# Performance work log

Measured on AMD Instinct MI355X. Metric: run time of the kernel, lower is better.

## Reference

```python
import jax, jax.numpy as jnp
import numpy as np

EPS = 1e-5
H = 8  # num_heads

def _bn(x, g, b):
    # training-mode BatchNorm over the LAST axis as channels; stats over all other axes
    axes = tuple(range(x.ndim - 1))
    mean = jnp.mean(x, axis=axes)
    var = jnp.var(x, axis=axes)  # biased, matches torch BN normalization
    return (x - mean) * jax.lax.rsqrt(var + EPS) * g + b


def setup_inputs() -> dict:
    key = jax.random.key(0)
    ks = jax.random.split(key, 16)
    m, S, C = 256, 128, 256
    s = 1.0 / np.sqrt(C)
    inp = {
        'x': jax.random.normal(ks[0], (m, S, C), jnp.float32),
        'g_n': jnp.ones((C,), jnp.float32), 'b_n': jnp.zeros((C,), jnp.float32),
        'Wq': jax.random.normal(ks[1], (C, C), jnp.float32) * s,
        'Wk': jax.random.normal(ks[2], (C, C), jnp.float32) * s,
        'Wv': jax.random.normal(ks[3], (C, C), jnp.float32) * s,
        'Wo': jax.random.normal(ks[4], (C, C), jnp.float32) * s,
        'bo': jnp.zeros((C,), jnp.float32),
        'g_pe': jnp.ones((S * S,), jnp.float32), 'b_pe': jnp.zeros((S * S,), jnp.float32),
        'g0': jnp.ones((C,), jnp.float32), 'b0': jnp.zeros((C,), jnp.float32),
        'W0': jax.random.normal(ks[5], (2 * C, C), jnp.float32) * s,
        'g1': jnp.ones((2 * C,), jnp.float32), 'b1': jnp.zeros((2 * C,), jnp.float32),
        'W1': jax.random.normal(ks[6], (C, 2 * C), jnp.float32) * (1.0 / np.sqrt(2 * C)),
    }
    return inp


def reference(x, g_n, b_n, Wq, Wk, Wv, Wo, bo, g_pe, b_pe, g0, b0, W0, g1, b1, W1):
    m, S, C = x.shape
    d = C // H
    # --- SelfAttention ---
    h = _bn(x, g_n, b_n)  # BN over channels C, stats over (batch, seq)
    q = (h @ Wq.T).reshape(m, S, H, d)
    k = (h @ Wk.T).reshape(m, S, H, d)
    v = (h @ Wv.T).reshape(m, S, H, d)
    energy = jnp.einsum('nqhc,nkhc->nhqk', q, k)  # [m,H,S,S]
    # BatchNorm1d over the flattened S*S 'channel' axis, stats over (batch, heads)
    e = energy.reshape(m, H, S * S)
    e = _bn(e, g_pe, b_pe)
    energy_post = e.reshape(m, H, S, S)
    attn = jax.nn.softmax(energy_post / jnp.sqrt(jnp.float32(C)), axis=-1)
    o = jnp.einsum('nhql,nlhc->nqhc', attn, v).reshape(m, S, C)
    x1 = o @ Wo.T + bo + x  # residual
    # --- FFN block ---
    out0 = _bn(x1, g0, b0)
    out1 = jax.nn.relu(out0)
    out2 = out1 @ W0.T            # [m,S,2C]
    out3 = _bn(out2, g1, b1)
    out4 = jax.nn.relu(out3)
    out5 = out4 @ W1.T            # [m,S,C]
    return x1 + out5  # dropout p=0.0 -> identity
```

## Files before the change

kernel.cpp:

```cpp
#include <hip/hip_runtime.h>
#include <hip/hip_bf16.h>

#define HH 8
#define SS 128
#define CC 256
#define DD 32
#define NTOK 32768
#define NHB 2048
#define BNEPS 1e-5f

using bf16 = __hip_bfloat16;
typedef float f32x4 __attribute__((ext_vector_type(4)));
typedef __bf16 bf16x8 __attribute__((ext_vector_type(8)));

__device__ __forceinline__ bf16x8 ld8(const bf16* p) {
    return *reinterpret_cast<const bf16x8*>(p);
}
__device__ __forceinline__ f32x4 ldf4(const float* p) {
    return *reinterpret_cast<const f32x4*>(p);
}
__device__ __forceinline__ void st8(bf16* p, bf16x8 v) {
    *reinterpret_cast<bf16x8*>(p) = v;
}
__device__ __forceinline__ bf16 bfc(__bf16 x) {
    union { __bf16 i; bf16 o; } u;
    u.i = x;
    return u.o;
}
__device__ __forceinline__ int swzg(int row, int g) {
    return ((g & 8) | ((g & 7) ^ (row & 7))) << 3;
}

typedef __attribute__((address_space(1))) const void g_void;
typedef __attribute__((address_space(3))) void l_void;
__device__ __forceinline__ void gload_lds16(const bf16* g, bf16* l) {
    __builtin_amdgcn_global_load_lds((g_void*)g, (l_void*)l, 16, 0, 0);
}

__global__ __launch_bounds__(256) void prep(const float* __restrict__ wq,
                                            const float* __restrict__ wk,
                                            const float* __restrict__ wv,
                                            const float* __restrict__ wo,
                                            const float* __restrict__ w0,
                                            const float* __restrict__ w1,
                                            bf16* __restrict__ out,
                                            const float* __restrict__ X,
                                            float* __restrict__ part) {
    int tid = threadIdx.x;
    if (blockIdx.x < 512) {
        int i = (blockIdx.x * 256 + tid) * 4;
        const float* src;
        int off;
        if (i < 65536) { src = wq; off = i; }
        else if (i < 131072) { src = wk; off = i - 65536; }
        else if (i < 196608) { src = wv; off = i - 131072; }
        else if (i < 262144) { src = wo; off = i - 196608; }
        else if (i < 393216) { src = w0; off = i - 262144; }
        else { src = w1; off = i - 393216; }
        f32x4 v = ldf4(src + off);
#pragma unroll
        for (int u = 0; u < 4; u++) out[i + u] = __float2bfloat16(v[u]);
        return;
    }
    int bx = blockIdx.x - 512;
    int cv = tid & 63, slot = tid >> 6;
    int c0 = cv * 4;
    size_t row0 = (size_t)bx * 256 + slot;
    float s[4], s2[4];
#pragma unroll
    for (int u = 0; u < 4; u++) { s[u] = 0.f; s2[u] = 0.f; }
    for (int i = 0; i < 64; i++) {
        size_t row = row0 + (size_t)i * 4;
        f32x4 v = ldf4(X + row * 256 + c0);
#pragma unroll
        for (int u = 0; u < 4; u++) {
            float f = v[u];
            s[u] += f; s2[u] += f * f;
        }
    }
    __shared__ float red[256][8];
#pragma unroll
    for (int u = 0; u < 4; u++) {
        red[tid][u] = s[u];
        red[tid][4 + u] = s2[u];
    }
    __syncthreads();
    if (tid < 64) {
#pragma unroll
        for (int sl = 1; sl < 4; sl++)
#pragma unroll
            for (int u = 0; u < 4; u++) {
                s[u] += red[tid + sl * 64][u];
                s2[u] += red[tid + sl * 64][4 + u];
            }
        float* dst = part + (size_t)bx * 512;
#pragma unroll
        for (int u = 0; u < 4; u++) {
            dst[c0 + u] = s[u];
            dst[256 + c0 + u] = s2[u];
        }
    }
}

template <int CH, int P, int ROWS>
__global__ __launch_bounds__(256) void statsA_wide(const bf16* __restrict__ X,
                                                   float* __restrict__ part) {
    constexpr int RB = ROWS / P;
    int c0 = (blockIdx.x * 256 + threadIdx.x) * 8;
    size_t row0 = (size_t)blockIdx.y * RB;
    float s[8], s2[8];
#pragma unroll
    for (int u = 0; u < 8; u++) { s[u] = 0.f; s2[u] = 0.f; }
    for (int i = 0; i < RB; i++) {
        bf16x8 v = ld8(X + (row0 + i) * CH + c0);
#pragma unroll
        for (int u = 0; u < 8; u++) {
            float f = (float)v[u];
            s[u] += f; s2[u] += f * f;
        }
    }
    float* dst = part + (size_t)blockIdx.y * (2 * CH);
#pragma unroll
    for (int u = 0; u < 8; u++) {
        dst[c0 + u] = s[u];
        dst[CH + c0 + u] = s2[u];
    }
}

__global__ __launch_bounds__(256) void statsB(const float* __restrict__ part, int P,
                                              int nch, float inv_n, float ps,
                                              const float* __restrict__ gamma,
                                              const float* __restrict__ beta,
                                              float* __restrict__ scale,
                                              float* __restrict__ bias) {
    int cl = threadIdx.x & 63, sl = threadIdx.x >> 6;
    int c = blockIdx.x * 64 + cl;
    float s = 0.f, s2 = 0.f;
    for (int p = sl; p < P; p += 4) {
        s += part[(size_t)p * 2 * nch + c];
        s2 += part[(size_t)p * 2 * nch + nch + c];
    }
    __shared__ float red[2][4][64];
    red[0][sl][cl] = s;
    red[1][sl][cl] = s2;
    __syncthreads();
    if (threadIdx.x < 64) {
        s = red[0][0][cl] + red[0][1][cl] + red[0][2][cl] + red[0][3][cl];
        s2 = red[1][0][cl] + red[1][1][cl] + red[1][2][cl] + red[1][3][cl];
        float mean = s * inv_n;
        float var = s2 * inv_n - mean * mean;
        float rstd = rsqrtf(var + BNEPS);
        float sc = gamma[c] * rstd;
        scale[c] = sc * ps;
        bias[c] = (beta[c] - mean * sc) * ps;
    }
}

template <int MODE, bool STATS, int ASRC>
__device__ __forceinline__ void gemm_core(
    const bf16* __restrict__ A, const float* __restrict__ Af,
    const bf16* __restrict__ B, int m0, int n0, int N, int K,
    const float* __restrict__ a_scale, const float* __restrict__ a_bias,
    const float* __restrict__ bias, const float* __restrict__ resf,
    bf16* __restrict__ outb, float* __restrict__ outf, float* __restrict__ spart,
    char* smem) {
    bf16* As = (bf16*)smem;
    bf16* Bs = As + 128 * 64;
    int tid = threadIdx.x;
    int lane = tid & 63, wave = tid >> 6;
    int quad = lane >> 4, l16 = lane & 15;
    int wm = (wave >> 1) * 64, wn = (wave & 1) * 64;
    int srow = lane >> 3;
    int scol = (lane & 7) * 8;
    int sgc = (((lane & 7) ^ srow) << 3);
    const bf16* Ab = (ASRC == 0) ? A + (size_t)m0 * K : A;
    const bf16* Bb = B + (size_t)n0 * K;
    f32x4 acc[4][4];
#pragma unroll
    for (int i = 0; i < 4; i++)
#pragma unroll
        for (int j = 0; j < 4; j++) acc[i][j] = f32x4{0.f, 0.f, 0.f, 0.f};

    for (int kt = 0; kt < K; kt += 64) {
        if (kt) __syncthreads();
#pragma unroll
        for (int i = 0; i < 4; i++) {
            int r = i * 32 + wave * 8;
            gload_lds16(Bb + (size_t)(r + srow) * K + kt + sgc, Bs + r * 64);
        }
        if (ASRC == 0) {
#pragma unroll
            for (int i = 0; i < 4; i++) {
                int r = i * 32 + wave * 8;
                gload_lds16(Ab + (size_t)(r + srow) * K + kt + sgc, As + r * 64);
            }
        } else {
            int c = kt + scol;
            f32x4 s0 = ldf4(a_scale + c), s1 = ldf4(a_scale + c + 4);
            f32x4 b0 = ldf4(a_bias + c), b1 = ldf4(a_bias + c + 4);
#pragma unroll
            for (int i = 0; i < 4; i++) {
                int r = i * 32 + wave * 8;
                size_t row = (size_t)(m0 + r + srow);
                bf16x8 av;
                if (ASRC == 3) {
                    bf16x8 xv = ld8(Ab + row * K + c);
#pragma unroll
                    for (int u = 0; u < 4; u++) {
                        float f = (float)xv[u] * s0[u] + b0[u];
                        f = fmaxf(f, 0.f);
                        av[u] = (__bf16)__float2bfloat16(f);
                    }
#pragma unroll
                    for (int u = 0; u < 4; u++) {
                        float f = (float)xv[u + 4] * s1[u] + b1[u];
                        f = fmaxf(f, 0.f);
                        av[u + 4] = (__bf16)__float2bfloat16(f);
                    }
                } else {
                    f32x4 x0 = ldf4(Af + row * K + c), x1v = ldf4(Af + row * K + c + 4);
#pragma unroll
                    for (int u = 0; u < 4; u++) {
                        float f = x0[u] * s0[u] + b0[u];
                        if (ASRC == 2) f = fmaxf(f, 0.f);
                        av[u] = (__bf16)__float2bfloat16(f);
                    }
#pragma unroll
                    for (int u = 0; u < 4; u++) {
                        float f = x1v[u] * s1[u] + b1[u];
                        if (ASRC == 2) f = fmaxf(f, 0.f);
                        av[u + 4] = (__bf16)__float2bfloat16(f);
                    }
                }
                st8(As + (r + srow) * 64 + sgc, av);
            }
        }
        __syncthreads();
#pragma unroll
        for (int ks = 0; ks < 2; ks++) {
#pragma unroll
            for (int uu = 0; uu < 1; uu++) {}
            bf16x8 af[4], bfr[4];
            int gq = ks * 4 + quad;
            int kb_ = ((gq ^ (l16 & 7)) << 3);
#pragma unroll
            for (int i = 0; i < 4; i++)
                af[i] = ld8(As + (wm + i * 16 + l16) * 64 + kb_);
#pragma unroll
            for (int j = 0; j < 4; j++)
                bfr[j] = ld8(Bs + (wn + j * 16 + l16) * 64 + kb_);
#pragma unroll
            for (int i = 0; i < 4; i++)
#pragma unroll
                for (int j = 0; j < 4; j++)
                    acc[i][j] = __builtin_amdgcn_mfma_f32_16x16x32_bf16(
                        af[i], bfr[j], acc[i][j], 0, 0, 0);
        }
    }
    __syncthreads();

    if (MODE == 0) {
        bf16(*Ct)[136] = (bf16(*)[136])smem;
#pragma unroll
        for (int i = 0; i < 4; i++)
#pragma unroll
            for (int j = 0; j < 4; j++)
#pragma unroll
                for (int r = 0; r < 4; r++)
                    Ct[wm + i * 16 + quad * 4 + r][wn + j * 16 + l16] =
                        __float2bfloat16(acc[i][j][r]);
        __syncthreads();
        float s[8], s2[8];
        if (STATS) {
#pragma unroll
            for (int u = 0; u < 8; u++) { s[u] = 0.f; s2[u] = 0.f; }
        }
#pragma unroll
        for (int it = 0; it < 8; it++) {
            int idx = it * 256 + tid;
            int row = idx >> 4, colv = idx & 15;
            bf16x8 c = ld8(&Ct[row][colv * 8]);
            st8(outb + (size_t)(m0 + row) * N + n0 + colv * 8, c);
            if (STATS) {
#pragma unroll
                for (int u = 0; u < 8; u++) {
                    float f = (float)c[u];
                    s[u] += f; s2[u] += f * f;
                }
            }
        }
        if (STATS) {
            __syncthreads();
            float* rf = (float*)smem;
            int g = tid & 15, k = tid >> 4;
#pragma unroll
            for (int u = 0; u < 8; u++) {
                rf[(g * 16 + k) * 16 + u] = s[u];
                rf[(g * 16 + k) * 16 + 8 + u] = s2[u];
            }
            __syncthreads();
            if (tid < 16) {
                float a[8], b[8];
#pragma unroll
                for (int u = 0; u < 8; u++) { a[u] = 0.f; b[u] = 0.f; }
                for (int k2 = 0; k2 < 16; k2++)
#pragma unroll
                    for (int u = 0; u < 8; u++) {
                        a[u] += rf[(tid * 16 + k2) * 16 + u];
                        b[u] += rf[(tid * 16 + k2) * 16 + 8 + u];
                    }
                float* dst = spart + (size_t)(m0 >> 7) * 2 * N + n0 + tid * 8;
#pragma unroll
                for (int u = 0; u < 8; u++) {
                    dst[u] = a[u];
                    dst[N + u] = b[u];
                }
            }
        }
    } else {
        float(*Cf)[132] = (float(*)[132])smem;
        float s[4], s2[4];
        if (STATS) {
#pragma unroll
            for (int u = 0; u < 4; u++) { s[u] = 0.f; s2[u] = 0.f; }
        }
#pragma unroll
        for (int h = 0; h < 2; h++) {
            if (h) __syncthreads();
            if ((wm >> 6) == h) {
#pragma unroll
                for (int i = 0; i < 4; i++)
#pragma unroll
                    for (int j = 0; j < 4; j++)
#pragma unroll
                        for (int r = 0; r < 4; r++)
                            Cf[i * 16 + quad * 4 + r][wn + j * 16 + l16] = acc[i][j][r];
            }
            __syncthreads();
#pragma unroll
            for (int it = 0; it < 8; it++) {
                int idx = it * 256 + tid;
                int row = idx >> 5, cv = (idx & 31) * 4;
                f32x4 v = ldf4(&Cf[row][cv]);
                int gc = n0 + cv;
                size_t gi = (size_t)(m0 + h * 64 + row) * N + gc;
                f32x4 rr = ldf4(resf + gi);
                if (MODE == 1) {
                    f32x4 bb = ldf4(bias + gc);
                    v = v + bb + rr;
                } else {
                    v = v + rr;
                }
                *reinterpret_cast<f32x4*>(outf + gi) = v;
                if (STATS) {
#pragma unroll
                    for (int u = 0; u < 4; u++) {
                        s[u] += v[u]; s2[u] += v[u] * v[u];
                    }
                }
            }
        }
        if (STATS) {
            __syncthreads();
            float* rf = (float*)smem;
            int g = tid & 31, k = tid >> 5;
#pragma unroll
            for (int u = 0; u < 4; u++) {
                rf[(g * 8 + k) * 8 + u] = s[u];
                rf[(g * 8 + k) * 8 + 4 + u] = s2[u];
            }
            __syncthreads();
            if (tid < 32) {
                float a[4], b[4];
#pragma unroll
                for (int u = 0; u < 4; u++) { a[u] = 0.f; b[u] = 0.f; }
                for (int k2 = 0; k2 < 8; k2++)
#pragma unroll
                    for (int u = 0; u < 4; u++) {
                        a[u] += rf[(tid * 8 + k2) * 8 + u];
                        b[u] += rf[(tid * 8 + k2) * 8 + 4 + u];
                    }
                float* dst = spart + (size_t)(m0 >> 7) * 2 * N + n0 + tid * 4;
#pragma unroll
                for (int u = 0; u < 4; u++) {
                    dst[u] = a[u];
                    dst[N + u] = b[u];
                }
            }
        }
    }
}

template <int MODE, bool STATS, int ASRC>
__global__ __launch_bounds__(256) void gemm128(
    const bf16* __restrict__ A, const float* __restrict__ Af,
    const bf16* __restrict__ B, int N, int K, const float* __restrict__ a_scale,
    const float* __restrict__ a_bias, const float* __restrict__ bias,
    const float* __restrict__ resf, bf16* __restrict__ outb,
    float* __restrict__ outf, float* __restrict__ spart) {
    __shared__ __align__(16) char smem[34816];
    gemm_core<MODE, STATS, ASRC>(A, Af, B, blockIdx.x * 128, blockIdx.y * 128, N, K,
                                 a_scale, a_bias, bias, resf, outb, outf, spart, smem);
}

__global__ __launch_bounds__(256) void gemm_qkv128(const float* __restrict__ x,
                                                   const bf16* __restrict__ W,
                                                   const float* __restrict__ a_scale,
                                                   const float* __restrict__ a_bias,
                                                   bf16* __restrict__ qkv) {
    __shared__ __align__(16) char smem[34816];
    int mat = blockIdx.y >> 1;
    int n0 = (blockIdx.y & 1) * 128;
    gemm_core<0, false, 1>(nullptr, x, W + mat * 65536, blockIdx.x * 128, n0, CC, CC,
                           a_scale, a_bias, nullptr, nullptr,
                           qkv + (size_t)mat * 8388608, nullptr, nullptr, smem);
}

__global__ __launch_bounds__(256) void gemm_energy(const bf16* __restrict__ q,
                                                   const bf16* __restrict__ k,
                                                   bf16* __restrict__ E) {
    int nh = blockIdx.x;
    int nb = nh >> 3, hh = nh & 7;
    int tid = threadIdx.x;
    int lane = tid & 63, wave = tid >> 6;
    int quad = lane >> 4, l16 = lane & 15;
    int wm = (wave >> 1) * 64, wn = (wave & 1) * 64;
    size_t tb = (size_t)nb * SS;
    int cb = hh * DD + quad * 8;
    f32x4 zero = {0.f, 0.f, 0.f, 0.f};
    f32x4 acc[4][4];
#pragma unroll
    for (int i = 0; i < 4; i++)
#pragma unroll
        for (int j = 0; j < 4; j++) acc[i][j] = zero;
    bf16x8 af[4], bfg[4];
#pragma unroll
    for (int i = 0; i < 4; i++)
        af[i] = ld8(q + (tb + wm + i * 16 + l16) * CC + cb);
#pragma unroll
    for (int j = 0; j < 4; j++)
        bfg[j] = ld8(k + (tb + wn + j * 16 + l16) * CC + cb);
#pragma unroll
    for (int i = 0; i < 4; i++)
#pragma unroll
        for (int j = 0; j < 4; j++)
            acc[i][j] = __builtin_amdgcn_mfma_f32_16x16x32_bf16(af[i], bfg[j], acc[i][j], 0, 0, 0);
    __shared__ bf16 Et[128][136];
#pragma unroll
    for (int i = 0; i < 4; i++)
#pragma unroll
        for (int j = 0; j < 4; j++)
#pragma unroll
            for (int r = 0; r < 4; r++)
                Et[wm + i * 16 + quad * 4 + r][wn + j * 16 + l16] =
                    __float2bfloat16(acc[i][j][r]);
    __syncthreads();
    bf16* Eb = E + (size_t)nh * SS * SS;
#pragma unroll
    for (int it = 0; it < 8; it++) {
        int idx = it * 256 + tid;
        int row = idx >> 4, colv = idx & 15;
        st8(Eb + (size_t)row * SS + colv * 8, ld8(&Et[row][colv * 8]));
    }
}

__global__ __launch_bounds__(256, 4) void att_kernel(
    const bf16* __restrict__ E, const bf16* __restrict__ v,
    const float* __restrict__ pe_scale, const float* __restrict__ pe_bias,
    bf16* __restrict__ o) {
    __shared__ bf16 P[SS * 128];
    __shared__ bf16 Vt[DD * 128];
    int nh = blockIdx.x;
    int nb = nh >> 3, hh = nh & 7;
    const bf16* Eb = E + (size_t)nh * SS * SS;
    int tid = threadIdx.x;
    int wave = tid >> 6, lane = tid & 63;
    {
        int s = tid >> 1, d0 = (tid & 1) * 16;
        const bf16* vp = v + (size_t)(nb * SS + s) * CC + hh * DD + d0;
        bf16x8 v0 = ld8(vp), v1 = ld8(vp + 8);
        int g = s >> 3, sub = s & 7;
#pragma unroll
        for (int u = 0; u < 8; u++) {
            int da = d0 + u, db = d0 + 8 + u;
            Vt[da * 128 + swzg(da, g) + sub] = bfc(v0[u]);
            Vt[db * 128 + swzg(db, g) + sub] = bfc(v1[u]);
        }
    }
    int rs = lane >> 4, cg = lane & 15;
#pragma unroll
    for (int p = 0; p < 8; p++) {
        int r = wave * 32 + p * 4 + rs;
        int e8 = r * 128 + cg * 8;
        bf16x8 ev = ld8(Eb + e8);
        f32x4 s0 = ldf4(pe_scale + e8), s1 = ldf4(pe_scale + e8 + 4);
        f32x4 b0 = ldf4(pe_bias + e8), b1 = ldf4(pe_bias + e8 + 4);
        float l[8];
#pragma unroll
        for (int u = 0; u < 4; u++) l[u] = (float)ev[u] * s0[u] + b0[u];
#pragma unroll
        for (int u = 0; u < 4; u++) l[u + 4] = (float)ev[u + 4] * s1[u] + b1[u];
        float mx = fmaxf(fmaxf(fmaxf(l[0], l[1]), fmaxf(l[2], l[3])),
                         fmaxf(fmaxf(l[4], l[5]), fmaxf(l[6], l[7])));
#pragma unroll
        for (int off = 8; off; off >>= 1) mx = fmaxf(mx, __shfl_xor(mx, off, 16));
        float e[8], sm = 0.f;
#pragma unroll
        for (int u = 0; u < 8; u++) { e[u] = __expf(l[u] - mx); sm += e[u]; }
#pragma unroll
        for (int off = 8; off; off >>= 1) sm += __shfl_xor(sm, off, 16);
        float inv = 1.0f / sm;
        bf16x8 pv;
#pragma unroll
        for (int u = 0; u < 8; u++) pv[u] = (__bf16)__float2bfloat16(e[u] * inv);
        st8(&P[r * 128 + swzg(r, cg)], pv);
    }
    __syncthreads();
    int quad = lane >> 4, l16 = lane & 15;
    f32x4 acc[2][2];
#pragma unroll
    for (int i = 0; i < 2; i++)
#pragma unroll
        for (int j = 0; j < 2; j++) acc[i][j] = f32x4{0.f, 0.f, 0.f, 0.f};
#pragma unroll
    for (int kk = 0; kk < SS; kk += 32) {
        int g = (kk >> 3) + quad;
        int r0 = wave * 32 + l16, r1 = r0 + 16;
        bf16x8 a0 = ld8(&P[r0 * 128 + swzg(r0, g)]);
        bf16x8 a1 = ld8(&P[r1 * 128 + swzg(r1, g)]);
        bf16x8 b0 = ld8(&Vt[l16 * 128 + swzg(l16, g)]);
        bf16x8 b1 = ld8(&Vt[(l16 + 16) * 128 + swzg(l16 + 16, g)]);
        acc[0][0] = __builtin_amdgcn_mfma_f32_16x16x32_bf16(a0, b0, acc[0][0], 0, 0, 0);
        acc[0][1] = __builtin_amdgcn_mfma_f32_16x16x32_bf16(a0, b1, acc[0][1], 0, 0, 0);
        acc[1][0] = __builtin_amdgcn_mfma_f32_16x16x32_bf16(a1, b0, acc[1][0], 0, 0, 0);
        acc[1][1] = __builtin_amdgcn_mfma_f32_16x16x32_bf16(a1, b1, acc[1][1], 0, 0, 0);
    }
    __syncthreads();
    bf16* Ob = P;
#pragma unroll
    for (int i = 0; i < 2; i++)
#pragma unroll
        for (int j = 0; j < 2; j++)
#pragma unroll
            for (int r = 0; r < 4; r++) {
                int row = wave * 32 + i * 16 + quad * 4 + r;
                int col = j * 16 + l16;
                Ob[row * 40 + col] = __float2bfloat16(acc[i][j][r]);
            }
    __syncthreads();
#pragma unroll
    for (int it = 0; it < 2; it++) {
        int idx = it * 256 + tid;
        int row = idx >> 2, colv = idx & 3;
        st8(o + (size_t)(nb * SS + row) * CC + hh * DD + colv * 8,
            ld8(&Ob[row * 40 + colv * 8]));
    }
}

#define WB_OFF 0u
#define O_OFF 1048576u
#define Q_OFF 17825792u
#define K_OFF 34603008u
#define VT_OFF 51380224u
#define E_OFF 68157440u
#define X1_OFF 17825792u
#define OUT2_OFF 68157440u

extern "C" void kernel_launch(void* const* d_in, const int* in_sizes, int n_in,
                              void* d_out, int out_size, void* d_ws, size_t ws_size,
                              hipStream_t stream) {
    const float* x = (const float*)d_in[0];
    const float* g_n = (const float*)d_in[1];
    const float* b_n = (const float*)d_in[2];
    const float* Wq = (const float*)d_in[3];
    const float* Wk = (const float*)d_in[4];
    const float* Wv = (const float*)d_in[5];
    const float* Wo = (const float*)d_in[6];
    const float* bo = (const float*)d_in[7];
    const float* g_pe = (const float*)d_in[8];
    const float* b_pe = (const float*)d_in[9];
    const float* g0 = (const float*)d_in[10];
    const float* b0 = (const float*)d_in[11];
    const float* W0 = (const float*)d_in[12];
    const float* g1 = (const float*)d_in[13];
    const float* b1 = (const float*)d_in[14];
    const float* W1 = (const float*)d_in[15];

    char* ws = (char*)d_ws;
    bf16* WB = (bf16*)(ws + WB_OFF);
    bf16* WOB = WB + 196608;
    bf16* W0B = WB + 262144;
    bf16* W1B = WB + 393216;
    bf16* qb = (bf16*)(ws + Q_OFF);
    bf16* kb = (bf16*)(ws + K_OFF);
    bf16* vb = (bf16*)(ws + VT_OFF);
    bf16* Ebuf = (bf16*)(ws + E_OFF);
    bf16* obuf = (bf16*)(ws + O_OFF);
    float* x1 = (float*)(ws + X1_OFF);
    bf16* out2 = (bf16*)(ws + OUT2_OFF);
    float* bn1_scale = (float*)(ws + E_OFF);
    float* bn1_bias = bn1_scale + 256;
    float* xpart = (float*)(ws + E_OFF + 65536);
    float* pe_scale = (float*)(ws + Q_OFF);
    float* pe_bias = pe_scale + 16384;
    float* pepart = (float*)(ws + Q_OFF + 131072);
    float* bn0_scale = (float*)(ws + O_OFF);
    float* bn0_bias = bn0_scale + 256;
    float* f1_scale = (float*)(ws + O_OFF + 4096);
    float* f1_bias = f1_scale + 512;
    float* x1part = (float*)(ws + VT_OFF);
    float* f1part = (float*)(ws + O_OFF + 16384);
    float* outp = (float*)d_out;

    prep<<<640, 256, 0, stream>>>(Wq, Wk, Wv, Wo, W0, W1, WB, x, xpart);
    statsB<<<4, 256, 0, stream>>>(xpart, 128, 256, 1.0f / 32768.0f, 1.0f, g_n, b_n,
                                  bn1_scale, bn1_bias);
    gemm_qkv128<<<dim3(256, 6), 256, 0, stream>>>(x, WB, bn1_scale, bn1_bias, qb);
    gemm_energy<<<NHB, 256, 0, stream>>>(qb, kb, Ebuf);
    statsA_wide<16384, 32, 2048><<<dim3(8, 32), 256, 0, stream>>>(Ebuf, pepart);
    statsB<<<256, 256, 0, stream>>>(pepart, 32, 16384, 1.0f / 2048.0f, 0.0625f, g_pe,
                                    b_pe, pe_scale, pe_bias);
    att_kernel<<<NHB, 256, 0, stream>>>(Ebuf, vb, pe_scale, pe_bias, obuf);
    gemm128<1, true, 0><<<dim3(256, 2), 256, 0, stream>>>(
        obuf, nullptr, WOB, CC, CC, nullptr, nullptr, bo, x, nullptr, x1, x1part);
    statsB<<<4, 256, 0, stream>>>(x1part, 256, 256, 1.0f / 32768.0f, 1.0f, g0, b0,
                                  bn0_scale, bn0_bias);
    gemm128<0, true, 2><<<dim3(256, 4), 256, 0, stream>>>(
        nullptr, x1, W0B, 2 * CC, CC, bn0_scale, bn0_bias, nullptr, nullptr, out2,
        nullptr, f1part);
    statsB<<<8, 256, 0, stream>>>(f1part, 256, 512, 1.0f / 32768.0f, 1.0f, g1, b1,
                                  f1_scale, f1_bias);
    gemm128<2, false, 3><<<dim3(256, 2), 256, 0, stream>>>(
        out2, nullptr, W1B, CC, 2 * CC, f1_scale, f1_bias, nullptr, x1, nullptr, outp,
        nullptr);
    (void)in_sizes; (void)n_in; (void)out_size; (void)ws_size;
    (void)kb; (void)vb;
}
```

Baseline: 320.1 us.

## Prefetch next A tile into registers during MFMA compute in GEMM K-loop

Restructures the GEMM K-loop into a two-step unrolled loop. The global loads of the next A tile (the fp32 or bf16 activations that are normalized in registers) are issued before the current tile's MFMA compute, using ping-pong register buffers. This hides global load latency behind the matrix math. The cost is extra register pressure from the double-buffered A fragments, which may lower occupancy, and the loop assumes K is a multiple of 128.

```diff
diff --git a/kernel.cpp b/kernel.cpp
--- a/kernel.cpp
+++ b/kernel.cpp
@@ -181,81 +181,114 @@
 #pragma unroll
         for (int j = 0; j < 4; j++) acc[i][j] = f32x4{0.f, 0.f, 0.f, 0.f};
 
-    for (int kt = 0; kt < K; kt += 64) {
-        if (kt) __syncthreads();
+    f32x4 ax0_a[4], ax1_a[4], ax0_b[4], ax1_b[4];
+    bf16x8 ab_a[4], ab_b[4];
+
+    auto pfetchA = [&](int kt, f32x4 (&ax0)[4], f32x4 (&ax1)[4], bf16x8 (&ab)[4]) {
+        int c = kt + scol;
+#pragma unroll
+        for (int i = 0; i < 4; i++) {
+            size_t row = (size_t)(m0 + i * 32 + wave * 8 + srow);
+            if (ASRC == 3) {
+                ab[i] = ld8(Ab + row * K + c);
+            } else {
+                ax0[i] = ldf4(Af + row * K + c);
+                ax1[i] = ldf4(Af + row * K + c + 4);
+            }
+        }
+    };
+    auto stageA = [&](int kt, f32x4 (&ax0)[4], f32x4 (&ax1)[4], bf16x8 (&ab)[4]) {
+        int c = kt + scol;
+        f32x4 s0 = ldf4(a_scale + c), s1 = ldf4(a_scale + c + 4);
+        f32x4 b0 = ldf4(a_bias + c), b1 = ldf4(a_bias + c + 4);
+#pragma unroll
+        for (int i = 0; i < 4; i++) {
+            int r = i * 32 + wave * 8;
+            bf16x8 av;
+            if (ASRC == 3) {
+#pragma unroll
+                for (int u = 0; u < 4; u++) {
+                    float f = (float)ab[i][u] * s0[u] + b0[u];
+                    f = fmaxf(f, 0.f);
+                    av[u] = (__bf16)__float2bfloat16(f);
+                }
+#pragma unroll
+                for (int u = 0; u < 4; u++) {
+                    float f = (float)ab[i][u + 4] * s1[u] + b1[u];
+                    f = fmaxf(f, 0.f);
+                    av[u + 4] = (__bf16)__float2bfloat16(f);
+                }
+            } else {
+#pragma unroll
+                for (int u = 0; u < 4; u++) {
+                    float f = ax0[i][u] * s0[u] + b0[u];
+                    if (ASRC == 2) f = fmaxf(f, 0.f);
+                    av[u] = (__bf16)__float2bfloat16(f);
+                }
+#pragma unroll
+                for (int u = 0; u < 4; u++) {
+                    float f = ax1[i][u] * s1[u] + b1[u];
+                    if (ASRC == 2) f = fmaxf(f, 0.f);
+                    av[u + 4] = (__bf16)__float2bfloat16(f);
+                }
+            }
+            st8(As + (r + srow) * 64 + sgc, av);
+        }
+    };
+    auto computeK = [&]() {
+#pragma unroll
+        for (int ks = 0; ks < 2; ks++) {
+            bf16x8 af[4], bfr[4];
+            int gq = ks * 4 + quad;
+            int kb_ = ((gq ^ (l16 & 7)) << 3);
+#pragma unroll
+            for (int i = 0; i < 4; i++)
+                af[i] = ld8(As + (wm + i * 16 + l16) * 64 + kb_);
+#pragma unroll
+            for (int j = 0; j < 4; j++)
+                bfr[j] = ld8(Bs + (wn + j * 16 + l16) * 64 + kb_);
+#pragma unroll
+            for (int i = 0; i < 4; i++)
+#pragma unroll
+                for (int j = 0; j < 4; j++)
+                    acc[i][j] = __builtin_amdgcn_mfma_f32_16x16x32_bf16(
+                        af[i], bfr[j], acc[i][j], 0, 0, 0);
+        }
+    };
+    auto stageB = [&](int kt) {
 #pragma unroll
         for (int i = 0; i < 4; i++) {
             int r = i * 32 + wave * 8;
             gload_lds16(Bb + (size_t)(r + srow) * K + kt + sgc, Bs + r * 64);
         }
-        if (ASRC == 0) {
-#pragma unroll
-            for (int i = 0; i < 4; i++) {
-                int r = i * 32 + wave * 8;
-                gload_lds16(Ab + (size_t)(r + srow) * K + kt + sgc, As + r * 64);
-            }
-        } else {
-            int c = kt + scol;
-            f32x4 s0 = ldf4(a_scale + c), s1 = ldf4(a_scale + c + 4);
-            f32x4 b0 = ldf4(a_bias + c), b1 = ldf4(a_bias + c + 4);
-#pragma unroll
-            for (int i = 0; i < 4; i++) {
-                int r = i * 32 + wave * 8;
-                size_t row = (size_t)(m0 + r + srow);
-                bf16x8 av;
-                if (ASRC == 3) {
-                    bf16x8 xv = ld8(Ab + row * K + c);
-#pragma unroll
-                    for (int u = 0; u < 4; u++) {
-                        float f = (float)xv[u] * s0[u] + b0[u];
-                        f = fmaxf(f, 0.f);
-                        av[u] = (__bf16)__float2bfloat16(f);
-                    }
-#pragma unroll
-                    for (int u = 0; u < 4; u++) {
-                        float f = (float)xv[u + 4] * s1[u] + b1[u];
-                        f = fmaxf(f, 0.f);
-                        av[u + 4] = (__bf16)__float2bfloat16(f);
-                    }
-                } else {
-                    f32x4 x0 = ldf4(Af + row * K + c), x1v = ldf4(Af + row * K + c + 4);
-#pragma unroll
-                    for (int u = 0; u < 4; u++) {
-                        float f = x0[u] * s0[u] + b0[u];
-                        if (ASRC == 2) f = fmaxf(f, 0.f);
-                        av[u] = (__bf16)__float2bfloat16(f);
-                    }
-#pragma unroll
-                    for (int u = 0; u < 4; u++) {
-                        float f = x1v[u] * s1[u] + b1[u];
-                        if (ASRC == 2) f = fmaxf(f, 0.f);
-                        av[u + 4] = (__bf16)__float2bfloat16(f);
-                    }
-                }
-                st8(As + (r + srow) * 64 + sgc, av);
-            }
-        }
+    };
+    auto stageAdirect = [&](int kt) {
+#pragma unroll
+        for (int i = 0; i < 4; i++) {
+            int r = i * 32 + wave * 8;
+            gload_lds16(Ab + (size_t)(r + srow) * K + kt + sgc, As + r * 64);
+        }
+    };
+
+    if (ASRC != 0) pfetchA(0, ax0_a, ax1_a, ab_a);
+    int nsteps = K >> 6;
+    for (int t = 0; t < nsteps; t += 2) {
+        int kt0 = t << 6, kt1 = kt0 + 64;
+        if (kt0) __syncthreads();
+        stageB(kt0);
+        if (ASRC == 0) stageAdirect(kt0);
+        else stageA(kt0, ax0_a, ax1_a, ab_a);
         __syncthreads();
-#pragma unroll
-        for (int ks = 0; ks < 2; ks++) {
-#pragma unroll
-            for (int uu = 0; uu < 1; uu++) {}
-            bf16x8 af[4], bfr[4];
-            int gq = ks * 4 + quad;
-            int kb_ = ((gq ^ (l16 & 7)) << 3);
-#pragma unroll
-            for (int i = 0; i < 4; i++)
-                af[i] = ld8(As + (wm + i * 16 + l16) * 64 + kb_);
-#pragma unroll
-            for (int j = 0; j < 4; j++)
-                bfr[j] = ld8(Bs + (wn + j * 16 + l16) * 64 + kb_);
-#pragma unroll
-            for (int i = 0; i < 4; i++)
-#pragma unroll
-                for (int j = 0; j < 4; j++)
-                    acc[i][j] = __builtin_amdgcn_mfma_f32_16x16x32_bf16(
-                        af[i], bfr[j], acc[i][j], 0, 0, 0);
-        }
+        if (ASRC != 0) pfetchA(kt1, ax0_b, ax1_b, ab_b);
+        computeK();
+        __syncthreads();
+        stageB(kt1);
+        if (ASRC == 0) stageAdirect(kt1);
+        else stageA(kt1, ax0_b, ax1_b, ab_b);
+        __syncthreads();
+        if (ASRC != 0 && t + 2 < nsteps)
+            pfetchA(kt1 + 64, ax0_a, ax1_a, ab_a);
+        computeK();
     }
     __syncthreads();
 
```

Result: slower. 326.8 us (+2.1%).

## Widen projection GEMM tiles to full 256-column N so each block covers all outputs

Applied to the files above, without the earlier changes.

Replaces the 128x128 GEMM core with a full-width variant where each block computes all 256 output columns. QKV and W0 use 128x256 tiles with 512 threads, and Wo and W1 use 64x256 tiles with 256 threads. The aim is to read and BN-transform each A row only once instead of once per N tile, cutting redundant A loads and normalization work. The residual epilogue now writes straight from registers rather than staging through LDS, which gives less coalesced stores. The larger tiles and thread counts may also lower occupancy.

```diff
diff --git a/kernel.cpp b/kernel.cpp
--- a/kernel.cpp
+++ b/kernel.cpp
@@ -156,25 +156,26 @@
     }
 }
 
-template <int MODE, bool STATS, int ASRC>
-__device__ __forceinline__ void gemm_core(
+template <int WM, int MODE, int ASRC, bool STATS>
+__device__ __forceinline__ void gemm256_core(
     const bf16* __restrict__ A, const float* __restrict__ Af,
     const bf16* __restrict__ B, int m0, int n0, int N, int K,
     const float* __restrict__ a_scale, const float* __restrict__ a_bias,
     const float* __restrict__ bias, const float* __restrict__ resf,
     bf16* __restrict__ outb, float* __restrict__ outf, float* __restrict__ spart,
     char* smem) {
+    constexpr int BM = WM * 64;
+    constexpr int NT = WM * 256;
+    constexpr int NB = 8 / WM;
     bf16* As = (bf16*)smem;
-    bf16* Bs = As + 128 * 64;
+    bf16* Bs = As + BM * 64;
     int tid = threadIdx.x;
     int lane = tid & 63, wave = tid >> 6;
     int quad = lane >> 4, l16 = lane & 15;
-    int wm = (wave >> 1) * 64, wn = (wave & 1) * 64;
+    int wm = (wave >> 2) * 64, wn = (wave & 3) * 64;
     int srow = lane >> 3;
-    int scol = (lane & 7) * 8;
     int sgc = (((lane & 7) ^ srow) << 3);
-    const bf16* Ab = (ASRC == 0) ? A + (size_t)m0 * K : A;
-    const bf16* Bb = B + (size_t)n0 * K;
+    const bf16* Ab = A + (size_t)m0 * K;
     f32x4 acc[4][4];
 #pragma unroll
     for (int i = 0; i < 4; i++)
@@ -184,27 +185,28 @@
     for (int kt = 0; kt < K; kt += 64) {
         if (kt) __syncthreads();
 #pragma unroll
-        for (int i = 0; i < 4; i++) {
-            int r = i * 32 + wave * 8;
-            gload_lds16(Bb + (size_t)(r + srow) * K + kt + sgc, Bs + r * 64);
+        for (int i = 0; i < NB; i++) {
+            int r = i * (NT / 8) + wave * 8;
+            gload_lds16(B + (size_t)(r + srow) * K + kt + sgc, Bs + r * 64);
         }
         if (ASRC == 0) {
 #pragma unroll
-            for (int i = 0; i < 4; i++) {
-                int r = i * 32 + wave * 8;
+            for (int i = 0; i < 2; i++) {
+                int r = i * (BM / 2) + wave * 8;
                 gload_lds16(Ab + (size_t)(r + srow) * K + kt + sgc, As + r * 64);
             }
         } else {
-            int c = kt + scol;
-            f32x4 s0 = ldf4(a_scale + c), s1 = ldf4(a_scale + c + 4);
-            f32x4 b0 = ldf4(a_bias + c), b1 = ldf4(a_bias + c + 4);
-#pragma unroll
-            for (int i = 0; i < 4; i++) {
-                int r = i * 32 + wave * 8;
-                size_t row = (size_t)(m0 + r + srow);
+#pragma unroll
+            for (int c = 0; c < 2; c++) {
+                int flat = c * NT + tid;
+                int row = flat >> 3, sl = flat & 7;
+                int col = kt + sl * 8;
+                f32x4 s0 = ldf4(a_scale + col), s1 = ldf4(a_scale + col + 4);
+                f32x4 b0 = ldf4(a_bias + col), b1 = ldf4(a_bias + col + 4);
+                size_t grow = (size_t)(m0 + row);
                 bf16x8 av;
                 if (ASRC == 3) {
-                    bf16x8 xv = ld8(Ab + row * K + c);
+                    bf16x8 xv = ld8(A + grow * K + col);
 #pragma unroll
                     for (int u = 0; u < 4; u++) {
                         float f = (float)xv[u] * s0[u] + b0[u];
@@ -218,7 +220,8 @@
                         av[u + 4] = (__bf16)__float2bfloat16(f);
                     }
                 } else {
-                    f32x4 x0 = ldf4(Af + row * K + c), x1v = ldf4(Af + row * K + c + 4);
+                    f32x4 x0 = ldf4(Af + grow * K + col);
+                    f32x4 x1v = ldf4(Af + grow * K + col + 4);
 #pragma unroll
                     for (int u = 0; u < 4; u++) {
                         float f = x0[u] * s0[u] + b0[u];
@@ -232,14 +235,12 @@
                         av[u + 4] = (__bf16)__float2bfloat16(f);
                     }
                 }
-                st8(As + (r + srow) * 64 + sgc, av);
+                st8(As + row * 64 + ((sl ^ (row & 7)) << 3), av);
             }
         }
         __syncthreads();
 #pragma unroll
         for (int ks = 0; ks < 2; ks++) {
-#pragma unroll
-            for (int uu = 0; uu < 1; uu++) {}
             bf16x8 af[4], bfr[4];
             int gq = ks * 4 + quad;
             int kb_ = ((gq ^ (l16 & 7)) << 3);
@@ -261,159 +262,163 @@
 
     if (MODE == 0) {
         bf16(*Ct)[136] = (bf16(*)[136])smem;
+        float s[2][8], s2[2][8];
+        if (STATS) {
+#pragma unroll
+            for (int h = 0; h < 2; h++)
+#pragma unroll
+                for (int u = 0; u < 8; u++) { s[h][u] = 0.f; s2[h][u] = 0.f; }
+        }
+#pragma unroll
+        for (int h = 0; h < 2; h++) {
+            if (h) __syncthreads();
+            if ((wn >> 7) == h) {
+#pragma unroll
+                for (int i = 0; i < 4; i++)
+#pragma unroll
+                    for (int j = 0; j < 4; j++)
+#pragma unroll
+                        for (int r = 0; r < 4; r++)
+                            Ct[wm + i * 16 + quad * 4 + r]
+                              [(wn & 127) + j * 16 + l16] =
+                                __float2bfloat16(acc[i][j][r]);
+            }
+            __syncthreads();
+#pragma unroll
+            for (int it = 0; it < 4; it++) {
+                int idx = it * NT + tid;
+                int row = idx >> 4, colv = tid & 15;
+                bf16x8 c = ld8(&Ct[row][colv * 8]);
+                st8(outb + (size_t)(m0 + row) * N + n0 + h * 128 + colv * 8, c);
+                if (STATS) {
+#pragma unroll
+                    for (int u = 0; u < 8; u++) {
+                        float f = (float)c[u];
+                        s[h][u] += f; s2[h][u] += f * f;
+                    }
+                }
+            }
+        }
+        if (STATS) {
+            float* sc = (float*)smem;
+#pragma unroll
+            for (int h = 0; h < 2; h++) {
+                __syncthreads();
+#pragma unroll
+                for (int u = 0; u < 8; u++) {
+                    sc[tid * 16 + u] = s[h][u];
+                    sc[tid * 16 + 8 + u] = s2[h][u];
+                }
+                __syncthreads();
+                if (tid < 128) {
+                    int cv = tid >> 3, u = tid & 7;
+                    float a = 0.f, b = 0.f;
+                    for (int k = 0; k < NT / 16; k++) {
+                        a += sc[(k * 16 + cv) * 16 + u];
+                        b += sc[(k * 16 + cv) * 16 + 8 + u];
+                    }
+                    int ch = n0 + h * 128 + cv * 8 + u;
+                    spart[(size_t)blockIdx.x * 2 * N + ch] = a;
+                    spart[(size_t)blockIdx.x * 2 * N + N + ch] = b;
+                }
+            }
+        }
+    } else {
+        float bo4[4];
+        if (MODE == 1) {
+#pragma unroll
+            for (int j = 0; j < 4; j++) bo4[j] = bias[wn + j * 16 + l16];
+        }
+        float s[4], s2[4];
+        if (STATS) {
+#pragma unroll
+            for (int j = 0; j < 4; j++) { s[j] = 0.f; s2[j] = 0.f; }
+        }
 #pragma unroll
         for (int i = 0; i < 4; i++)
 #pragma unroll
             for (int j = 0; j < 4; j++)
 #pragma unroll
-                for (int r = 0; r < 4; r++)
-                    Ct[wm + i * 16 + quad * 4 + r][wn + j * 16 + l16] =
-                        __float2bfloat16(acc[i][j][r]);
-        __syncthreads();
-        float s[8], s2[8];
-        if (STATS) {
-#pragma unroll
-            for (int u = 0; u < 8; u++) { s[u] = 0.f; s2[u] = 0.f; }
-        }
-#pragma unroll
-        for (int it = 0; it < 8; it++) {
-            int idx = it * 256 + tid;
-            int row = idx >> 4, colv = idx & 15;
-            bf16x8 c = ld8(&Ct[row][colv * 8]);
-            st8(outb + (size_t)(m0 + row) * N + n0 + colv * 8, c);
-            if (STATS) {
-#pragma unroll
-                for (int u = 0; u < 8; u++) {
-                    float f = (float)c[u];
-                    s[u] += f; s2[u] += f * f;
+                for (int r = 0; r < 4; r++) {
+                    int rg = m0 + i * 16 + quad * 4 + r;
+                    int col = wn + j * 16 + l16;
+                    size_t gi = (size_t)rg * 256 + col;
+                    float v = acc[i][j][r] + resf[gi];
+                    if (MODE == 1) v += bo4[j];
+                    outf[gi] = v;
+                    if (STATS) { s[j] += v; s2[j] += v * v; }
                 }
-            }
-        }
         if (STATS) {
             __syncthreads();
-            float* rf = (float*)smem;
-            int g = tid & 15, k = tid >> 4;
-#pragma unroll
-            for (int u = 0; u < 8; u++) {
-                rf[(g * 16 + k) * 16 + u] = s[u];
-                rf[(g * 16 + k) * 16 + 8 + u] = s2[u];
+            float* sc = (float*)smem;
+#pragma unroll
+            for (int j = 0; j < 4; j++) {
+                sc[tid * 8 + j] = s[j];
+                sc[tid * 8 + 4 + j] = s2[j];
             }
             __syncthreads();
-            if (tid < 16) {
-                float a[8], b[8];
-#pragma unroll
-                for (int u = 0; u < 8; u++) { a[u] = 0.f; b[u] = 0.f; }
-                for (int k2 = 0; k2 < 16; k2++)
-#pragma unroll
-                    for (int u = 0; u < 8; u++) {
-                        a[u] += rf[(tid * 16 + k2) * 16 + u];
-                        b[u] += rf[(tid * 16 + k2) * 16 + 8 + u];
-                    }
-                float* dst = spart + (size_t)(m0 >> 7) * 2 * N + n0 + tid * 8;
-#pragma unroll
-                for (int u = 0; u < 8; u++) {
-                    dst[u] = a[u];
-                    dst[N + u] = b[u];
+            {
+                int w = tid >> 6, j = (tid >> 4) & 3, l = tid & 15;
+                float a = 0.f, b = 0.f;
+#pragma unroll
+                for (int q = 0; q < 4; q++) {
+                    a += sc[(w * 64 + q * 16 + l) * 8 + j];
+                    b += sc[(w * 64 + q * 16 + l) * 8 + 4 + j];
                 }
-            }
-        }
-    } else {
-        float(*Cf)[132] = (float(*)[132])smem;
-        float s[4], s2[4];
-        if (STATS) {
-#pragma unroll
-            for (int u = 0; u < 4; u++) { s[u] = 0.f; s2[u] = 0.f; }
-        }
-#pragma unroll
-        for (int h = 0; h < 2; h++) {
-            if (h) __syncthreads();
-            if ((wm >> 6) == h) {
-#pragma unroll
-                for (int i = 0; i < 4; i++)
-#pragma unroll
-                    for (int j = 0; j < 4; j++)
-#pragma unroll
-                        for (int r = 0; r < 4; r++)
-                            Cf[i * 16 + quad * 4 + r][wn + j * 16 + l16] = acc[i][j][r];
-            }
-            __syncthreads();
-#pragma unroll
-            for (int it = 0; it < 8; it++) {
-                int idx = it * 256 + tid;
-                int row = idx >> 5, cv = (idx & 31) * 4;
-                f32x4 v = ldf4(&Cf[row][cv]);
-                int gc = n0 + cv;
-                size_t gi = (size_t)(m0 + h * 64 + row) * N + gc;
-                f32x4 rr = ldf4(resf + gi);
-                if (MODE == 1) {
-                    f32x4 bb = ldf4(bias + gc);
-                    v = v + bb + rr;
-                } else {
-                    v = v + rr;
-                }
-                *reinterpret_cast<f32x4*>(outf + gi) = v;
-                if (STATS) {
-#pragma unroll
-                    for (int u = 0; u < 4; u++) {
-                        s[u] += v[u]; s2[u] += v[u] * v[u];
-                    }
-                }
-            }
-        }
-        if (STATS) {
-            __syncthreads();
-            float* rf = (float*)smem;
-            int g = tid & 31, k = tid >> 5;
-#pragma unroll
-            for (int u = 0; u < 4; u++) {
-                rf[(g * 8 + k) * 8 + u] = s[u];
-                rf[(g * 8 + k) * 8 + 4 + u] = s2[u];
-            }
-            __syncthreads();
-            if (tid < 32) {
-                float a[4], b[4];
-#pragma unroll
-                for (int u = 0; u < 4; u++) { a[u] = 0.f; b[u] = 0.f; }
-                for (int k2 = 0; k2 < 8; k2++)
-#pragma unroll
-                    for (int u = 0; u < 4; u++) {
-                        a[u] += rf[(tid * 8 + k2) * 8 + u];
-                        b[u] += rf[(tid * 8 + k2) * 8 + 4 + u];
-                    }
-                float* dst = spart + (size_t)(m0 >> 7) * 2 * N + n0 + tid * 4;
-#pragma unroll
-                for (int u = 0; u < 4; u++) {
-                    dst[u] = a[u];
-                    dst[N + u] = b[u];
-                }
-            }
-        }
-    }
-}
-
-template <int MODE, bool STATS, int ASRC>
-__global__ __launch_bounds__(256) void gemm128(
-    const bf16* __restrict__ A, const float* __restrict__ Af,
-    const bf16* __restrict__ B, int N, int K, const float* __restrict__ a_scale,
-    const float* __restrict__ a_bias, const float* __restrict__ bias,
-    const float* __restrict__ resf, bf16* __restrict__ outb,
-    float* __restrict__ outf, float* __restrict__ spart) {
-    __shared__ __align__(16) char smem[34816];
-    gemm_core<MODE, STATS, ASRC>(A, Af, B, blockIdx.x * 128, blockIdx.y * 128, N, K,
-                                 a_scale, a_bias, bias, resf, outb, outf, spart, smem);
-}
-
-__global__ __launch_bounds__(256) void gemm_qkv128(const float* __restrict__ x,
-                                                   const bf16* __restrict__ W,
-                                                   const float* __restrict__ a_scale,
-                                                   const float* __restrict__ a_bias,
-                                                   bf16* __restrict__ qkv) {
-    __shared__ __align__(16) char smem[34816];
-    int mat = blockIdx.y >> 1;
-    int n0 = (blockIdx.y & 1) * 128;
-    gemm_core<0, false, 1>(nullptr, x, W + mat * 65536, blockIdx.x * 128, n0, CC, CC,
-                           a_scale, a_bias, nullptr, nullptr,
-                           qkv + (size_t)mat * 8388608, nullptr, nullptr, smem);
+                int ch = w * 64 + j * 16 + l;
+                spart[(size_t)blockIdx.x * 512 + ch] = a;
+                spart[(size_t)blockIdx.x * 512 + 256 + ch] = b;
+            }
+        }
+    }
+}
+
+__global__ __launch_bounds__(512) void qkv256(const float* __restrict__ x,
+                                              const bf16* __restrict__ W,
+                                              const float* __restrict__ a_scale,
+                                              const float* __restrict__ a_bias,
+                                              bf16* __restrict__ qkv) {
+    __shared__ __align__(16) char smem[49152];
+    int mat = blockIdx.y;
+    gemm256_core<2, 0, 1, false>(nullptr, x, W + mat * 65536, blockIdx.x * 128, 0, 256,
+                                 256, a_scale, a_bias, nullptr, nullptr,
+                                 qkv + (size_t)mat * 8388608, nullptr, nullptr, smem);
+}
+
+__global__ __launch_bounds__(256) void gemmWo(const bf16* __restrict__ obuf,
+                                              const bf16* __restrict__ W,
+                                              const float* __restrict__ bo,
+                                              const float* __restrict__ x,
+                                              float* __restrict__ x1,
+                                              float* __restrict__ spart) {
+    __shared__ __align__(16) char smem[40960];
+    gemm256_core<1, 1, 0, true>(obuf, nullptr, W, blockIdx.x * 64, 0, 256, 256,
+                                nullptr, nullptr, bo, x, nullptr, x1, spart, smem);
+}
+
+__global__ __launch_bounds__(512) void gemmW0(const float* __restrict__ x1,
+                                              const bf16* __restrict__ W,
+                                              const float* __restrict__ a_scale,
+                                              const float* __restrict__ a_bias,
+                                              bf16* __restrict__ out2,
+                                              float* __restrict__ spart) {
+    __shared__ __align__(16) char smem[49152];
+    int n0 = blockIdx.y * 256;
+    gemm256_core<2, 0, 2, true>(nullptr, x1, W + (size_t)n0 * 256, blockIdx.x * 128,
+                                n0, 512, 256, a_scale, a_bias, nullptr, nullptr, out2,
+                                nullptr, spart, smem);
+}
+
+__global__ __launch_bounds__(256) void gemmW1(const bf16* __restrict__ out2,
+                                              const bf16* __restrict__ W,
+                                              const float* __restrict__ a_scale,
+                                              const float* __restrict__ a_bias,
+                                              const float* __restrict__ x1,
+                                              float* __restrict__ outp) {
+    __shared__ __align__(16) char smem[40960];
+    gemm256_core<1, 2, 3, false>(out2, nullptr, W, blockIdx.x * 64, 0, 256, 512,
+                                 a_scale, a_bias, nullptr, x1, nullptr, outp, nullptr,
+                                 smem);
 }
 
 __global__ __launch_bounds__(256) void gemm_energy(const bf16* __restrict__ q,
@@ -615,24 +620,20 @@
     prep<<<640, 256, 0, stream>>>(Wq, Wk, Wv, Wo, W0, W1, WB, x, xpart);
     statsB<<<4, 256, 0, stream>>>(xpart, 128, 256, 1.0f / 32768.0f, 1.0f, g_n, b_n,
                                   bn1_scale, bn1_bias);
-    gemm_qkv128<<<dim3(256, 6), 256, 0, stream>>>(x, WB, bn1_scale, bn1_bias, qb);
+    qkv256<<<dim3(256, 3), 512, 0, stream>>>(x, WB, bn1_scale, bn1_bias, qb);
     gemm_energy<<<NHB, 256, 0, stream>>>(qb, kb, Ebuf);
     statsA_wide<16384, 32, 2048><<<dim3(8, 32), 256, 0, stream>>>(Ebuf, pepart);
     statsB<<<256, 256, 0, stream>>>(pepart, 32, 16384, 1.0f / 2048.0f, 0.0625f, g_pe,
                                     b_pe, pe_scale, pe_bias);
     att_kernel<<<NHB, 256, 0, stream>>>(Ebuf, vb, pe_scale, pe_bias, obuf);
-    gemm128<1, true, 0><<<dim3(256, 2), 256, 0, stream>>>(
-        obuf, nullptr, WOB, CC, CC, nullptr, nullptr, bo, x, nullptr, x1, x1part);
-    statsB<<<4, 256, 0, stream>>>(x1part, 256, 256, 1.0f / 32768.0f, 1.0f, g0, b0,
+    gemmWo<<<512, 256, 0, stream>>>(obuf, WOB, bo, x, x1, x1part);
+    statsB<<<4, 256, 0, stream>>>(x1part, 512, 256, 1.0f / 32768.0f, 1.0f, g0, b0,
                                   bn0_scale, bn0_bias);
-    gemm128<0, true, 2><<<dim3(256, 4), 256, 0, stream>>>(
-        nullptr, x1, W0B, 2 * CC, CC, bn0_scale, bn0_bias, nullptr, nullptr, out2,
-        nullptr, f1part);
+    gemmW0<<<dim3(256, 2), 512, 0, stream>>>(x1, W0B, bn0_scale, bn0_bias, out2,
+                                             f1part);
     statsB<<<8, 256, 0, stream>>>(f1part, 256, 512, 1.0f / 32768.0f, 1.0f, g1, b1,
                                   f1_scale, f1_bias);
-    gemm128<2, false, 3><<<dim3(256, 2), 256, 0, stream>>>(
-        out2, nullptr, W1B, CC, 2 * CC, f1_scale, f1_bias, nullptr, x1, nullptr, outp,
-        nullptr);
+    gemmW1<<<512, 256, 0, stream>>>(out2, W1B, f1_scale, f1_bias, x1, outp);
     (void)in_sizes; (void)n_in; (void)out_size; (void)ws_size;
     (void)kb; (void)vb;
 }
```

New measurement: 338.4 us. 5.7% more time.
